# Performance work log

Hardware: AMD Instinct MI355X
Metric: run time of the kernel (lower is better)

The kernel has to match this reference:

```python
import jax, jax.numpy as jnp
import numpy as np

B, N, D, DS, LAT, FD, NF = 2, 384, 128, 3, 256, 1, 2
NPOS = DS * (2 * 5 + 1)  # 3 + 3*2*5 = 33
FREQS = np.linspace(1.0, 32.0, 5)  # torch.linspace(1, 2**5, 5)
EPS = 1e-5


def _bn(x, g, b):
    # BatchNorm1d, train-mode batch stats: normalize per channel over (batch, points)
    m = jnp.mean(x, axis=(0, 1))
    v = jnp.var(x, axis=(0, 1))
    return (x - m) * jax.lax.rsqrt(v + EPS) * g + b


def _tblock(xyz4, f, Wq, Wk, Wv, Wg1, bg1, Wg2, bg2, Wpe, bpe, g, b):
    # group_all=True full vector attention. f: [B,n,D], xyz4: [B,n,3]
    q = f @ Wq.T
    k = f @ Wk.T
    v = f @ Wv.T
    # knn_xyz gathered under no_grad in torch -> stop_gradient on the key side
    pd = xyz4[:, :, None] - jax.lax.stop_gradient(xyz4)[:, None]  # [B,n,n,3]
    parts = [pd]
    for fr in FREQS:
        parts.append(jnp.sin(pd * fr))
        parts.append(jnp.cos(pd * fr))
    pos = jnp.concatenate(parts, axis=-1) @ Wpe.T + bpe  # [B,n,n,D]
    edges = q[:, :, None] - k[:, None] + pos  # [B,n,n,D]
    h = jax.nn.relu(edges @ Wg1.T + bg1)
    attn = jax.nn.softmax(h @ Wg2.T + bg2, axis=-2)  # softmax over neighbor axis
    res = jnp.sum(attn * (v[:, None] + pos), axis=2)  # einsum bmnf,bmnf->bmf
    return _bn(res + f, g, b)


def setup_inputs() -> dict:
    key = jax.random.key(0)
    ks = iter(jax.random.split(key, 40))
    def rn(shape, s=0.05):
        return jax.random.normal(next(ks), shape, dtype=jnp.float32) * s
    z = lambda *s: jnp.zeros(s, jnp.float32)
    o = lambda *s: jnp.ones(s, jnp.float32)
    nb = NF + 1  # begin block + nfinal blocks
    return {
        "xyz": jax.random.normal(next(ks), (B, N, DS), dtype=jnp.float32),
        "feats": jax.random.normal(next(ks), (B, N, FD), dtype=jnp.float32),
        "enc_W": rn((D, FD)), "enc_b": z(D),
        "tb_Wq": rn((nb, D, D)), "tb_Wk": rn((nb, D, D)), "tb_Wv": rn((nb, D, D)),
        "tb_Wg1": rn((nb, D, D)), "tb_bg1": z(nb, D),
        "tb_Wg2": rn((nb, D, D)), "tb_bg2": z(nb, D),
        "tb_Wpe": rn((nb, D, NPOS)), "tb_bpe": z(nb, D),
        "tb_gamma": o(nb, D), "tb_beta": z(nb, D),
        "em_W1": rn((NF, D, D)), "em_b1": z(NF, D),
        "em_W2": rn((NF, D, D)), "em_b2": z(NF, D),
        "em_gamma": o(NF, D), "em_beta": z(NF, D),
        "fcf_W1": rn((LAT, D)), "fcf_b1": z(LAT),
        "fcf_W2": rn((LAT, LAT)), "fcf_b2": z(LAT),
    }


def reference(xyz, feats, enc_W, enc_b, tb_Wq, tb_Wk, tb_Wv, tb_Wg1, tb_bg1,
              tb_Wg2, tb_bg2, tb_Wpe, tb_bpe, tb_gamma, tb_beta,
              em_W1, em_b1, em_W2, em_b2, em_gamma, em_beta,
              fcf_W1, fcf_b1, fcf_W2, fcf_b2):
    f = feats @ enc_W.T + enc_b  # enc_feats
    x4 = xyz * 4.0
    for i in range(NF + 1):  # i=0: transformer_begin; i>=1: final transformers
        f = _tblock(x4, f, tb_Wq[i], tb_Wk[i], tb_Wv[i], tb_Wg1[i], tb_bg1[i],
                    tb_Wg2[i], tb_bg2[i], tb_Wpe[i], tb_bpe[i], tb_gamma[i], tb_beta[i])
        if i > 0:
            j = i - 1  # ElementwiseMLP: bn(x + relu(conv2(relu(conv1(x)))))
            y = jax.nn.relu(f @ em_W1[j].T + em_b1[j])
            y = jax.nn.relu(y @ em_W2[j].T + em_b2[j])
            f = _bn(f + y, em_gamma[j], em_beta[j])
    e = jax.nn.relu(f @ fcf_W1.T + fcf_b1) @ fcf_W2.T + fcf_b2
    return jnp.max(e, axis=1)  # lat_rep [B, lat_dim]
```

## Files before the change

kernel.cpp:

```cpp
#include <hip/hip_runtime.h>
#include <hip/hip_bf16.h>

#define B_ 2
#define N_ 384
#define D_ 128
#define LAT_ 256
#define NPOS_ 33
#define ROWS_ (B_*N_)
#define NT_ 64
#define ITERS_ (N_/NT_)

typedef __attribute__((ext_vector_type(8))) short bf16x8;
typedef __attribute__((ext_vector_type(4))) float f32x4;

#define MFMA(a,b,c) __builtin_amdgcn_mfma_f32_16x16x32_bf16((a),(b),(c),0,0,0)

__device__ __forceinline__ unsigned short f2bf(float x) {
    unsigned int u = __float_as_uint(x);
    u += 0x7FFFu + ((u >> 16) & 1u);
    return (unsigned short)(u >> 16);
}

__device__ __forceinline__ float bn_apply(float x, const float* stats, const float* gam,
                                          const float* bet, int d) {
    float s  = stats[d], sq = stats[128 + d];
    float mean = s * (1.f/ROWS_);
    float var  = sq * (1.f/ROWS_) - mean*mean;
    return (x - mean) * rsqrtf(var + 1e-5f) * gam[d] + bet[d];
}

__global__ __launch_bounds__(256) void enc_kernel(const float* __restrict__ feats,
                           const float* __restrict__ W,
                           const float* __restrict__ bias,
                           float* __restrict__ f) {
    int i = blockIdx.x*256 + threadIdx.x;
    if (i >= ROWS_*D_) return;
    int r = i >> 7, d = i & 127;
    f[i] = feats[r]*W[d] + bias[d];
}

__global__ __launch_bounds__(128) void qkv_kernel(const float* __restrict__ graw,
    const float* __restrict__ stats, const float* __restrict__ gam, const float* __restrict__ bet,
    int use_stats,
    const float* __restrict__ Wq, const float* __restrict__ Wk, const float* __restrict__ Wv,
    float* __restrict__ q, float* __restrict__ k, float* __restrict__ v) {
    __shared__ float row[D_];
    int r = blockIdx.x, d = threadIdx.x;
    float x = graw[r*D_+d];
    if (use_stats) x = bn_apply(x, stats, gam, bet, d);
    row[d] = x;
    __syncthreads();
    float aq=0.f, ak=0.f, av=0.f;
    #pragma unroll 4
    for (int e4=0;e4<D_/4;e4++){
        float4 wq = *(const float4*)(Wq + d*D_ + e4*4);
        float4 wk = *(const float4*)(Wk + d*D_ + e4*4);
        float4 wv = *(const float4*)(Wv + d*D_ + e4*4);
        float x0=row[e4*4+0], x1=row[e4*4+1], x2=row[e4*4+2], x3=row[e4*4+3];
        aq += wq.x*x0 + wq.y*x1 + wq.z*x2 + wq.w*x3;
        ak += wk.x*x0 + wk.y*x1 + wk.z*x2 + wk.w*x3;
        av += wv.x*x0 + wv.y*x1 + wv.z*x2 + wv.w*x3;
    }
    q[r*D_+d]=aq; k[r*D_+d]=ak; v[r*D_+d]=av;
}

__global__ __launch_bounds__(512) void attn_mfma_kernel(
    const float* __restrict__ xyz, const float* __restrict__ graw,
    const float* __restrict__ stats_in, const float* __restrict__ gam_in,
    const float* __restrict__ bet_in, int use_stats,
    const float* __restrict__ qb, const float* __restrict__ kb, const float* __restrict__ vb,
    const float* __restrict__ Wpe, const float* __restrict__ bpe,
    const float* __restrict__ Wg1, const float* __restrict__ bg1,
    const float* __restrict__ Wg2, const float* __restrict__ bg2,
    float* __restrict__ gout, float* __restrict__ stats_out)
{
    __shared__ unsigned short sParts[NT_*64];
    __shared__ unsigned short sX[NT_*128];
    __shared__ unsigned short sH[NT_*128];
    __shared__ float sRed[4*128];

    const int t   = threadIdx.x;
    const int w   = t >> 6;
    const int l   = t & 63;
    const int lr  = l & 15;
    const int lg  = l >> 4;
    const int rb2 = w >> 2;
    const int ct0 = (w & 3) * 2;

    const int row  = blockIdx.x;
    const int b    = row / N_;
    const int brow = b * N_;

    bf16x8 bWg1[2][4], bWg2[2][4], bWpe[2][2];
    float  bpe_c[2], bg1_c[2], bg2_c[2], q_c[2];

    #pragma unroll
    for (int ct = 0; ct < 2; ++ct) {
        const int dout = (ct0 + ct) * 16 + lr;
        #pragma unroll
        for (int kt = 0; kt < 4; ++kt) {
            const float* p1 = Wg1 + dout * D_ + kt * 32 + lg * 8;
            const float* p2 = Wg2 + dout * D_ + kt * 32 + lg * 8;
            float4 a0 = *(const float4*)(p1);
            float4 a1 = *(const float4*)(p1 + 4);
            float4 c0 = *(const float4*)(p2);
            float4 c1 = *(const float4*)(p2 + 4);
            bf16x8 v1, v2;
            v1[0]=(short)f2bf(a0.x); v1[1]=(short)f2bf(a0.y); v1[2]=(short)f2bf(a0.z); v1[3]=(short)f2bf(a0.w);
            v1[4]=(short)f2bf(a1.x); v1[5]=(short)f2bf(a1.y); v1[6]=(short)f2bf(a1.z); v1[7]=(short)f2bf(a1.w);
            v2[0]=(short)f2bf(c0.x); v2[1]=(short)f2bf(c0.y); v2[2]=(short)f2bf(c0.z); v2[3]=(short)f2bf(c0.w);
            v2[4]=(short)f2bf(c1.x); v2[5]=(short)f2bf(c1.y); v2[6]=(short)f2bf(c1.z); v2[7]=(short)f2bf(c1.w);
            bWg1[ct][kt] = v1;
            bWg2[ct][kt] = v2;
        }
        #pragma unroll
        for (int kt = 0; kt < 2; ++kt) {
            bf16x8 vv;
            #pragma unroll
            for (int e = 0; e < 8; ++e) {
                const int p = kt*32 + lg*8 + e;
                const float x = (p < NPOS_) ? Wpe[dout*NPOS_ + p] : 0.f;
                vv[e] = (short)f2bf(x);
            }
            bWpe[ct][kt] = vv;
        }
        bpe_c[ct] = bpe[dout];
        bg1_c[ct] = bg1[dout];
        bg2_c[ct] = bg2[dout];
        q_c[ct]   = qb[row*D_ + dout];
    }

    const float x4m0 = 4.f*xyz[row*3+0];
    const float x4m1 = 4.f*xyz[row*3+1];
    const float x4m2 = 4.f*xyz[row*3+2];

    for (int i = t; i < NT_*64/2; i += 512) ((unsigned int*)sParts)[i] = 0u;
    __syncthreads();

    auto partsgen = [&](int n0) {
        const int rr = t >> 3, j = t & 7;
        const int nr = (brow + n0 + rr) * 3;
        const float pd0 = x4m0 - 4.f*xyz[nr+0];
        const float pd1 = x4m1 - 4.f*xyz[nr+1];
        const float pd2 = x4m2 - 4.f*xyz[nr+2];
        auto pval = [&](int p) -> float {
            if (p < 3) return p==0?pd0:(p==1?pd1:pd2);
            const int qq = p - 3;
            const int fi = qq / 6;
            int rem = qq - fi*6;
            bool is_sin = true;
            if (rem >= 3) { rem -= 3; is_sin = false; }
            const float pdj = rem==0?pd0:(rem==1?pd1:pd2);
            const float fr = fi==0?1.f:(fi==1?8.75f:(fi==2?16.5f:(fi==3?24.25f:32.f)));
            const float a = pdj * fr;
            return is_sin ? __sinf(a) : __cosf(a);
        };
        const int sw = (rr & 7) << 3;
        #pragma unroll
        for (int k8 = 0; k8 < 4; ++k8) {
            const int p = j + k8*8;
            sParts[(rr*64 + p) ^ sw] = f2bf(pval(p));
        }
        if (j == 0) sParts[(rr*64 + 32) ^ sw] = f2bf(pval(32));
    };

    float kreg[2][2][4], vreg[2][2][4];
    auto loadK = [&](int n0) {
        #pragma unroll
        for (int rt = 0; rt < 2; ++rt)
        #pragma unroll
        for (int ct = 0; ct < 2; ++ct) {
            const int d = (ct0 + ct)*16 + lr;
            #pragma unroll
            for (int r = 0; r < 4; ++r) {
                const int rr = rb2*32 + rt*16 + lg*4 + r;
                kreg[rt][ct][r] = kb[(brow + n0 + rr)*D_ + d];
            }
        }
    };
    auto loadV = [&](int n0) {
        #pragma unroll
        for (int rt = 0; rt < 2; ++rt)
        #pragma unroll
        for (int ct = 0; ct < 2; ++ct) {
            const int d = (ct0 + ct)*16 + lr;
            #pragma unroll
            for (int r = 0; r < 4; ++r) {
                const int rr = rb2*32 + rt*16 + lg*4 + r;
                vreg[rt][ct][r] = vb[(brow + n0 + rr)*D_ + d];
            }
        }
    };

    f32x4 pos[2][2];
    auto posedges = [&]() {
        #pragma unroll
        for (int rt = 0; rt < 2; ++rt)
        #pragma unroll
        for (int ct = 0; ct < 2; ++ct) {
            f32x4 acc = {0.f, 0.f, 0.f, 0.f};
            #pragma unroll
            for (int kt = 0; kt < 2; ++kt) {
                const int r16 = rb2*32 + rt*16 + lr;
                const int idx = (r16*64 + kt*32 + lg*8) ^ ((r16 & 7) << 3);
                bf16x8 a = *(const bf16x8*)&sParts[idx];
                acc = MFMA(a, bWpe[ct][kt], acc);
            }
            #pragma unroll
            for (int r = 0; r < 4; ++r) acc[r] += bpe_c[ct];
            pos[rt][ct] = acc;
        }
        #pragma unroll
        for (int rt = 0; rt < 2; ++rt)
        #pragma unroll
        for (int ct = 0; ct < 2; ++ct) {
            const int d = (ct0 + ct)*16 + lr;
            #pragma unroll
            for (int r = 0; r < 4; ++r) {
                const int rr = rb2*32 + rt*16 + lg*4 + r;
                const float e = pos[rt][ct][r] + q_c[ct] - kreg[rt][ct][r];
                sX[(rr*128 + d) ^ ((rr & 7) << 3)] = f2bf(e);
            }
        }
    };

    partsgen(0);
    __syncthreads();
    loadK(0);
    posedges();
    __syncthreads();

    float res_p[2] = {0.f, 0.f}, s_p[2] = {0.f, 0.f};

    for (int it = 0; it < ITERS_; ++it) {
        const int n0 = it * NT_;
        const bool more = (it < ITERS_ - 1);

        loadV(n0);
        f32x4 hacc[2][2];
        #pragma unroll
        for (int rt = 0; rt < 2; ++rt) {
            hacc[rt][0] = (f32x4){bg1_c[0], bg1_c[0], bg1_c[0], bg1_c[0]};
            hacc[rt][1] = (f32x4){bg1_c[1], bg1_c[1], bg1_c[1], bg1_c[1]};
            #pragma unroll
            for (int kt = 0; kt < 4; ++kt) {
                const int r16 = rb2*32 + rt*16 + lr;
                const int idx = (r16*128 + kt*32 + lg*8) ^ ((r16 & 7) << 3);
                bf16x8 a = *(const bf16x8*)&sX[idx];
                hacc[rt][0] = MFMA(a, bWg1[0][kt], hacc[rt][0]);
                hacc[rt][1] = MFMA(a, bWg1[1][kt], hacc[rt][1]);
            }
        }
        #pragma unroll
        for (int rt = 0; rt < 2; ++rt)
        #pragma unroll
        for (int ct = 0; ct < 2; ++ct) {
            const int d = (ct0 + ct)*16 + lr;
            #pragma unroll
            for (int r = 0; r < 4; ++r) {
                const int rr = rb2*32 + rt*16 + lg*4 + r;
                sH[(rr*128 + d) ^ ((rr & 7) << 3)] = f2bf(fmaxf(hacc[rt][ct][r], 0.f));
            }
        }
        __syncthreads();

        if (more) loadK(n0 + NT_);
        f32x4 lacc[2][2];
        #pragma unroll
        for (int rt = 0; rt < 2; ++rt) {
            lacc[rt][0] = (f32x4){bg2_c[0], bg2_c[0], bg2_c[0], bg2_c[0]};
            lacc[rt][1] = (f32x4){bg2_c[1], bg2_c[1], bg2_c[1], bg2_c[1]};
            #pragma unroll
            for (int kt = 0; kt < 4; ++kt) {
                const int r16 = rb2*32 + rt*16 + lr;
                const int idx = (r16*128 + kt*32 + lg*8) ^ ((r16 & 7) << 3);
                bf16x8 a = *(const bf16x8*)&sH[idx];
                lacc[rt][0] = MFMA(a, bWg2[0][kt], lacc[rt][0]);
                lacc[rt][1] = MFMA(a, bWg2[1][kt], lacc[rt][1]);
            }
        }
        #pragma unroll
        for (int rt = 0; rt < 2; ++rt)
        #pragma unroll
        for (int ct = 0; ct < 2; ++ct) {
            #pragma unroll
            for (int r = 0; r < 4; ++r) {
                const float wgt = __expf(lacc[rt][ct][r]);
                const float vp  = vreg[rt][ct][r] + pos[rt][ct][r];
                res_p[ct] += wgt * vp;
                s_p[ct]   += wgt;
            }
        }
        if (more) partsgen(n0 + NT_);
        __syncthreads();

        if (more) {
            posedges();
            __syncthreads();
        }
    }

    #pragma unroll
    for (int ct = 0; ct < 2; ++ct) {
        #pragma unroll
        for (int off = 16; off < 64; off <<= 1) {
            res_p[ct] += __shfl_xor(res_p[ct], off, 64);
            s_p[ct]   += __shfl_xor(s_p[ct], off, 64);
        }
    }
    if (lg == 0) {
        #pragma unroll
        for (int ct = 0; ct < 2; ++ct) {
            const int d = (ct0 + ct)*16 + lr;
            sRed[(rb2*2+0)*128 + d] = res_p[ct];
            sRed[(rb2*2+1)*128 + d] = s_p[ct];
        }
    }
    __syncthreads();
    if (t < D_) {
        const float rsum = sRed[t]       + sRed[2*128 + t];
        const float ssum = sRed[128 + t] + sRed[3*128 + t];
        float fres = graw[row*D_ + t];
        if (use_stats) fres = bn_apply(fres, stats_in, gam_in, bet_in, t);
        const float val = rsum / ssum + fres;
        gout[row*D_ + t] = val;
        atomicAdd(&stats_out[t], val);
        atomicAdd(&stats_out[128 + t], val*val);
    }
}

__global__ __launch_bounds__(128) void em_kernel(const float* __restrict__ graw,
    const float* __restrict__ stats_in, const float* __restrict__ gam_in, const float* __restrict__ bet_in,
    const float* __restrict__ W1, const float* __restrict__ b1,
    const float* __restrict__ W2, const float* __restrict__ b2,
    float* __restrict__ gout, float* __restrict__ stats_out)
{
    __shared__ float row[D_], y1[D_];
    int r = blockIdx.x, d = threadIdx.x;
    float fn = bn_apply(graw[r*D_+d], stats_in, gam_in, bet_in, d);
    row[d] = fn; __syncthreads();
    float a = b1[d];
    #pragma unroll 4
    for (int e4=0;e4<D_/4;e4++){
        float4 w = *(const float4*)(W1 + d*D_ + e4*4);
        a += w.x*row[e4*4+0] + w.y*row[e4*4+1] + w.z*row[e4*4+2] + w.w*row[e4*4+3];
    }
    y1[d] = fmaxf(a,0.f); __syncthreads();
    float a2 = b2[d];
    #pragma unroll 4
    for (int e4=0;e4<D_/4;e4++){
        float4 w = *(const float4*)(W2 + d*D_ + e4*4);
        a2 += w.x*y1[e4*4+0] + w.y*y1[e4*4+1] + w.z*y1[e4*4+2] + w.w*y1[e4*4+3];
    }
    a2 = fmaxf(a2,0.f);
    const float g2 = fn + a2;
    gout[r*D_+d] = g2;
    atomicAdd(&stats_out[d], g2);
    atomicAdd(&stats_out[128+d], g2*g2);
}

__global__ __launch_bounds__(256) void final_kernel(const float* __restrict__ graw,
    const float* __restrict__ stats_in, const float* __restrict__ gam_in, const float* __restrict__ bet_in,
    const float* __restrict__ W1, const float* __restrict__ b1,
    const float* __restrict__ W2, const float* __restrict__ b2,
    float* __restrict__ e_ws)
{
    __shared__ float row[D_];
    __shared__ float h1[LAT_];
    int r = blockIdx.x, t = threadIdx.x;
    if (t < D_) row[t] = bn_apply(graw[r*D_+t], stats_in, gam_in, bet_in, t);
    __syncthreads();
    float a = b1[t];
    #pragma unroll 4
    for (int e4=0;e4<D_/4;e4++){
        float4 w = *(const float4*)(W1 + t*D_ + e4*4);
        a += w.x*row[e4*4+0] + w.y*row[e4*4+1] + w.z*row[e4*4+2] + w.w*row[e4*4+3];
    }
    h1[t] = fmaxf(a,0.f);
    __syncthreads();
    float a2 = b2[t];
    #pragma unroll 4
    for (int e4=0;e4<LAT_/4;e4++){
        float4 w = *(const float4*)(W2 + t*LAT_ + e4*4);
        a2 += w.x*h1[e4*4+0] + w.y*h1[e4*4+1] + w.z*h1[e4*4+2] + w.w*h1[e4*4+3];
    }
    e_ws[r*LAT_+t] = a2;
}

__global__ __launch_bounds__(256) void maxred_kernel(const float* __restrict__ e_ws,
                                                     float* __restrict__ out)
{
    int b = blockIdx.x, l = threadIdx.x;
    float m = -INFINITY;
    #pragma unroll 8
    for (int n=0;n<N_;n++) m = fmaxf(m, e_ws[(b*N_+n)*LAT_+l]);
    out[b*LAT_+l] = m;
}

extern "C" void kernel_launch(void* const* d_in, const int* in_sizes, int n_in,
                              void* d_out, int out_size, void* d_ws, size_t ws_size,
                              hipStream_t stream) {
    (void)in_sizes; (void)n_in; (void)out_size; (void)ws_size;
    const float* xyz    = (const float*)d_in[0];
    const float* feats  = (const float*)d_in[1];
    const float* enc_W  = (const float*)d_in[2];
    const float* enc_b  = (const float*)d_in[3];
    const float* tb_Wq  = (const float*)d_in[4];
    const float* tb_Wk  = (const float*)d_in[5];
    const float* tb_Wv  = (const float*)d_in[6];
    const float* tb_Wg1 = (const float*)d_in[7];
    const float* tb_bg1 = (const float*)d_in[8];
    const float* tb_Wg2 = (const float*)d_in[9];
    const float* tb_bg2 = (const float*)d_in[10];
    const float* tb_Wpe = (const float*)d_in[11];
    const float* tb_bpe = (const float*)d_in[12];
    const float* tb_gamma = (const float*)d_in[13];
    const float* tb_beta  = (const float*)d_in[14];
    const float* em_W1  = (const float*)d_in[15];
    const float* em_b1  = (const float*)d_in[16];
    const float* em_W2  = (const float*)d_in[17];
    const float* em_b2  = (const float*)d_in[18];
    const float* em_gamma = (const float*)d_in[19];
    const float* em_beta  = (const float*)d_in[20];
    const float* fcf_W1 = (const float*)d_in[21];
    const float* fcf_b1 = (const float*)d_in[22];
    const float* fcf_W2 = (const float*)d_in[23];
    const float* fcf_b2 = (const float*)d_in[24];
    float* out = (float*)d_out;

    float* ws   = (float*)d_ws;
    float* buf0 = ws;
    float* buf1 = buf0 + ROWS_*D_;
    float* qbuf = buf1 + ROWS_*D_;
    float* kbuf = qbuf + ROWS_*D_;
    float* vbuf = kbuf + ROWS_*D_;
    float* ebuf = vbuf + ROWS_*D_;
    float* stats = ebuf + ROWS_*LAT_;
    float* sA0 = stats;
    float* sA1 = stats + 256;
    float* sE1 = stats + 512;
    float* sA2 = stats + 768;
    float* sE2 = stats + 1024;

    hipMemsetAsync(stats, 0, 5*256*sizeof(float), stream);

    enc_kernel<<<(ROWS_*D_+255)/256, 256, 0, stream>>>(feats, enc_W, enc_b, buf0);

    const float* gz = tb_gamma;
    qkv_kernel<<<ROWS_, 128, 0, stream>>>(buf0, gz, gz, gz, 0,
                                          tb_Wq, tb_Wk, tb_Wv, qbuf, kbuf, vbuf);
    attn_mfma_kernel<<<ROWS_, 512, 0, stream>>>(xyz, buf0, gz, gz, gz, 0,
        qbuf, kbuf, vbuf,
        tb_Wpe, tb_bpe, tb_Wg1, tb_bg1, tb_Wg2, tb_bg2, buf1, sA0);
    qkv_kernel<<<ROWS_, 128, 0, stream>>>(buf1, sA0, tb_gamma, tb_beta, 1,
                                          tb_Wq + 1*D_*D_, tb_Wk + 1*D_*D_, tb_Wv + 1*D_*D_,
                                          qbuf, kbuf, vbuf);
    attn_mfma_kernel<<<ROWS_, 512, 0, stream>>>(xyz, buf1, sA0, tb_gamma, tb_beta, 1,
        qbuf, kbuf, vbuf,
        tb_Wpe + 1*D_*NPOS_, tb_bpe + 1*D_, tb_Wg1 + 1*D_*D_, tb_bg1 + 1*D_,
        tb_Wg2 + 1*D_*D_, tb_bg2 + 1*D_, buf0, sA1);
    em_kernel<<<ROWS_, 128, 0, stream>>>(buf0, sA1, tb_gamma + 1*D_, tb_beta + 1*D_,
                                         em_W1, em_b1, em_W2, em_b2, buf1, sE1);
    qkv_kernel<<<ROWS_, 128, 0, stream>>>(buf1, sE1, em_gamma, em_beta, 1,
                                          tb_Wq + 2*D_*D_, tb_Wk + 2*D_*D_, tb_Wv + 2*D_*D_,
                                          qbuf, kbuf, vbuf);
    attn_mfma_kernel<<<ROWS_, 512, 0, stream>>>(xyz, buf1, sE1, em_gamma, em_beta, 1,
        qbuf, kbuf, vbuf,
        tb_Wpe + 2*D_*NPOS_, tb_bpe + 2*D_, tb_Wg1 + 2*D_*D_, tb_bg1 + 2*D_,
        tb_Wg2 + 2*D_*D_, tb_bg2 + 2*D_, buf0, sA2);
    em_kernel<<<ROWS_, 128, 0, stream>>>(buf0, sA2, tb_gamma + 2*D_, tb_beta + 2*D_,
                                         em_W1 + 1*D_*D_, em_b1 + 1*D_,
                                         em_W2 + 1*D_*D_, em_b2 + 1*D_, buf1, sE2);
    final_kernel<<<ROWS_, 256, 0, stream>>>(buf1, sE2, em_gamma + 1*D_, em_beta + 1*D_,
                                            fcf_W1, fcf_b1, fcf_W2, fcf_b2, ebuf);
    maxred_kernel<<<B_, 256, 0, stream>>>(ebuf, out);
}
```

Measured before the change: 607.6 us.

## Factor positional sin/cos encoding via angle addition and precompute per-point features

Uses the angle-addition identities to split sin/cos(f*(xm-xn)) into per-point sin/cos features of the neighbour, computed once by a new prep kernel, and folds the query-side terms into per-row MFMA weights. This removes per-tile transcendental generation and one barrier from the attention loop. K and V are stored as bf16 to halve their loads, and the K prefetch moves earlier. The qkv, em and final kernels now process four rows per block to reuse weight loads. Accuracy may change slightly because the folded weights are rounded to bf16 after combining with the query-side sin/cos.

```diff
diff --git a/kernel.cpp b/kernel.cpp
--- a/kernel.cpp
+++ b/kernel.cpp
@@ -20,6 +20,9 @@
     u += 0x7FFFu + ((u >> 16) & 1u);
     return (unsigned short)(u >> 16);
 }
+__device__ __forceinline__ float bf2f(unsigned short u) {
+    return __uint_as_float(((unsigned int)u) << 16);
+}
 
 __device__ __forceinline__ float bn_apply(float x, const float* stats, const float* gam,
                                           const float* bet, int d) {
@@ -27,6 +30,23 @@
     float mean = s * (1.f/ROWS_);
     float var  = sq * (1.f/ROWS_) - mean*mean;
     return (x - mean) * rsqrtf(var + 1e-5f) * gam[d] + bet[d];
+}
+
+__global__ __launch_bounds__(256) void fprep_kernel(const float* __restrict__ xyz,
+                                                    unsigned short* __restrict__ gF) {
+    int i = blockIdx.x*256 + threadIdx.x;
+    if (i >= ROWS_*64) return;
+    int n = i >> 6, q = i & 63;
+    float val;
+    if (q == 0) val = 1.f;
+    else if (q < 4) val = 4.f*xyz[n*3 + (q-1)];
+    else if (q < 34) {
+        int u = q-4, fi = u/6, rem = u - fi*6, j = rem >> 1;
+        const float fr = fi==0?1.f:(fi==1?8.75f:(fi==2?16.5f:(fi==3?24.25f:32.f)));
+        float a = fr*4.f*xyz[n*3+j];
+        val = (rem & 1) ? __sinf(a) : __cosf(a);
+    } else val = 0.f;
+    gF[n*64 + (q ^ ((n & 7) << 3))] = f2bf(val);
 }
 
 __global__ __launch_bounds__(256) void enc_kernel(const float* __restrict__ feats,
@@ -43,38 +63,51 @@
     const float* __restrict__ stats, const float* __restrict__ gam, const float* __restrict__ bet,
     int use_stats,
     const float* __restrict__ Wq, const float* __restrict__ Wk, const float* __restrict__ Wv,
-    float* __restrict__ q, float* __restrict__ k, float* __restrict__ v) {
-    __shared__ float row[D_];
-    int r = blockIdx.x, d = threadIdx.x;
-    float x = graw[r*D_+d];
-    if (use_stats) x = bn_apply(x, stats, gam, bet, d);
-    row[d] = x;
-    __syncthreads();
-    float aq=0.f, ak=0.f, av=0.f;
+    float* __restrict__ q, unsigned short* __restrict__ k16, unsigned short* __restrict__ v16) {
+    __shared__ float rows[4][D_];
+    const int r0 = blockIdx.x*4, d = threadIdx.x;
+    #pragma unroll
+    for (int rr = 0; rr < 4; ++rr) {
+        float x = graw[(r0+rr)*D_ + d];
+        if (use_stats) x = bn_apply(x, stats, gam, bet, d);
+        rows[rr][d] = x;
+    }
+    __syncthreads();
+    float aq[4] = {0,0,0,0}, ak[4] = {0,0,0,0}, av[4] = {0,0,0,0};
     #pragma unroll 4
-    for (int e4=0;e4<D_/4;e4++){
+    for (int e4 = 0; e4 < D_/4; ++e4) {
         float4 wq = *(const float4*)(Wq + d*D_ + e4*4);
         float4 wk = *(const float4*)(Wk + d*D_ + e4*4);
         float4 wv = *(const float4*)(Wv + d*D_ + e4*4);
-        float x0=row[e4*4+0], x1=row[e4*4+1], x2=row[e4*4+2], x3=row[e4*4+3];
-        aq += wq.x*x0 + wq.y*x1 + wq.z*x2 + wq.w*x3;
-        ak += wk.x*x0 + wk.y*x1 + wk.z*x2 + wk.w*x3;
-        av += wv.x*x0 + wv.y*x1 + wv.z*x2 + wv.w*x3;
-    }
-    q[r*D_+d]=aq; k[r*D_+d]=ak; v[r*D_+d]=av;
+        #pragma unroll
+        for (int rr = 0; rr < 4; ++rr) {
+            float4 x = *(const float4*)&rows[rr][e4*4];
+            aq[rr] += wq.x*x.x + wq.y*x.y + wq.z*x.z + wq.w*x.w;
+            ak[rr] += wk.x*x.x + wk.y*x.y + wk.z*x.z + wk.w*x.w;
+            av[rr] += wv.x*x.x + wv.y*x.y + wv.z*x.z + wv.w*x.w;
+        }
+    }
+    #pragma unroll
+    for (int rr = 0; rr < 4; ++rr) {
+        q[(r0+rr)*D_ + d]   = aq[rr];
+        k16[(r0+rr)*D_ + d] = f2bf(ak[rr]);
+        v16[(r0+rr)*D_ + d] = f2bf(av[rr]);
+    }
 }
 
 __global__ __launch_bounds__(512) void attn_mfma_kernel(
     const float* __restrict__ xyz, const float* __restrict__ graw,
     const float* __restrict__ stats_in, const float* __restrict__ gam_in,
     const float* __restrict__ bet_in, int use_stats,
-    const float* __restrict__ qb, const float* __restrict__ kb, const float* __restrict__ vb,
+    const float* __restrict__ qb,
+    const unsigned short* __restrict__ kb, const unsigned short* __restrict__ vb,
+    const unsigned short* __restrict__ gF,
     const float* __restrict__ Wpe, const float* __restrict__ bpe,
     const float* __restrict__ Wg1, const float* __restrict__ bg1,
     const float* __restrict__ Wg2, const float* __restrict__ bg2,
     float* __restrict__ gout, float* __restrict__ stats_out)
 {
-    __shared__ unsigned short sParts[NT_*64];
+    __shared__ unsigned short sF[NT_*64];
     __shared__ unsigned short sX[NT_*128];
     __shared__ unsigned short sH[NT_*128];
     __shared__ float sRed[4*128];
@@ -91,8 +124,43 @@
     const int b    = row / N_;
     const int brow = b * N_;
 
-    bf16x8 bWg1[2][4], bWg2[2][4], bWpe[2][2];
-    float  bpe_c[2], bg1_c[2], bg2_c[2], q_c[2];
+    uint4 fst = *(const uint4*)(gF + (size_t)brow*64 + t*8);
+
+    float kreg[2][2][4], vreg[2][2][4];
+    auto loadK = [&](int n0) {
+        #pragma unroll
+        for (int rt = 0; rt < 2; ++rt)
+        #pragma unroll
+        for (int ct = 0; ct < 2; ++ct) {
+            const int d = (ct0 + ct)*16 + lr;
+            #pragma unroll
+            for (int r = 0; r < 4; ++r) {
+                const int rr = rb2*32 + rt*16 + lg*4 + r;
+                kreg[rt][ct][r] = bf2f(kb[(brow + n0 + rr)*D_ + d]);
+            }
+        }
+    };
+    auto loadV = [&](int n0) {
+        #pragma unroll
+        for (int rt = 0; rt < 2; ++rt)
+        #pragma unroll
+        for (int ct = 0; ct < 2; ++ct) {
+            const int d = (ct0 + ct)*16 + lr;
+            #pragma unroll
+            for (int r = 0; r < 4; ++r) {
+                const int rr = rb2*32 + rt*16 + lg*4 + r;
+                vreg[rt][ct][r] = bf2f(vb[(brow + n0 + rr)*D_ + d]);
+            }
+        }
+    };
+    loadK(0);
+
+    bf16x8 bWg1[2][4], bWg2[2][4], bG[2][2];
+    float  bg1_c[2], bg2_c[2], q_c[2];
+
+    const float xm0 = 4.f*xyz[row*3+0];
+    const float xm1 = 4.f*xyz[row*3+1];
+    const float xm2 = 4.f*xyz[row*3+2];
 
     #pragma unroll
     for (int ct = 0; ct < 2; ++ct) {
@@ -113,85 +181,35 @@
             bWg1[ct][kt] = v1;
             bWg2[ct][kt] = v2;
         }
+        const float* wrow = Wpe + dout*NPOS_;
+        float bias = bpe[dout] + wrow[0]*xm0 + wrow[1]*xm1 + wrow[2]*xm2;
         #pragma unroll
         for (int kt = 0; kt < 2; ++kt) {
-            bf16x8 vv;
+            bf16x8 g;
             #pragma unroll
             for (int e = 0; e < 8; ++e) {
-                const int p = kt*32 + lg*8 + e;
-                const float x = (p < NPOS_) ? Wpe[dout*NPOS_ + p] : 0.f;
-                vv[e] = (short)f2bf(x);
-            }
-            bWpe[ct][kt] = vv;
-        }
-        bpe_c[ct] = bpe[dout];
+                const int qq = kt*32 + lg*8 + e;
+                float val;
+                if (qq == 0) val = bias;
+                else if (qq < 4) val = -wrow[qq-1];
+                else if (qq < 34) {
+                    const int u = qq - 4, fi = u/6, rem = u - fi*6, j = rem >> 1;
+                    const float Ws = wrow[3 + 6*fi + j];
+                    const float Wc = wrow[3 + 6*fi + 3 + j];
+                    const float fr = fi==0?1.f:(fi==1?8.75f:(fi==2?16.5f:(fi==3?24.25f:32.f)));
+                    const float am = fr * (j==0?xm0:(j==1?xm1:xm2));
+                    const float sm = __sinf(am), cm = __cosf(am);
+                    val = (rem & 1) ? (Wc*sm - Ws*cm) : (Ws*sm + Wc*cm);
+                } else val = 0.f;
+                g[e] = (short)f2bf(val);
+            }
+            bG[ct][kt] = g;
+        }
         bg1_c[ct] = bg1[dout];
         bg2_c[ct] = bg2[dout];
         q_c[ct]   = qb[row*D_ + dout];
     }
 
-    const float x4m0 = 4.f*xyz[row*3+0];
-    const float x4m1 = 4.f*xyz[row*3+1];
-    const float x4m2 = 4.f*xyz[row*3+2];
-
-    for (int i = t; i < NT_*64/2; i += 512) ((unsigned int*)sParts)[i] = 0u;
-    __syncthreads();
-
-    auto partsgen = [&](int n0) {
-        const int rr = t >> 3, j = t & 7;
-        const int nr = (brow + n0 + rr) * 3;
-        const float pd0 = x4m0 - 4.f*xyz[nr+0];
-        const float pd1 = x4m1 - 4.f*xyz[nr+1];
-        const float pd2 = x4m2 - 4.f*xyz[nr+2];
-        auto pval = [&](int p) -> float {
-            if (p < 3) return p==0?pd0:(p==1?pd1:pd2);
-            const int qq = p - 3;
-            const int fi = qq / 6;
-            int rem = qq - fi*6;
-            bool is_sin = true;
-            if (rem >= 3) { rem -= 3; is_sin = false; }
-            const float pdj = rem==0?pd0:(rem==1?pd1:pd2);
-            const float fr = fi==0?1.f:(fi==1?8.75f:(fi==2?16.5f:(fi==3?24.25f:32.f)));
-            const float a = pdj * fr;
-            return is_sin ? __sinf(a) : __cosf(a);
-        };
-        const int sw = (rr & 7) << 3;
-        #pragma unroll
-        for (int k8 = 0; k8 < 4; ++k8) {
-            const int p = j + k8*8;
-            sParts[(rr*64 + p) ^ sw] = f2bf(pval(p));
-        }
-        if (j == 0) sParts[(rr*64 + 32) ^ sw] = f2bf(pval(32));
-    };
-
-    float kreg[2][2][4], vreg[2][2][4];
-    auto loadK = [&](int n0) {
-        #pragma unroll
-        for (int rt = 0; rt < 2; ++rt)
-        #pragma unroll
-        for (int ct = 0; ct < 2; ++ct) {
-            const int d = (ct0 + ct)*16 + lr;
-            #pragma unroll
-            for (int r = 0; r < 4; ++r) {
-                const int rr = rb2*32 + rt*16 + lg*4 + r;
-                kreg[rt][ct][r] = kb[(brow + n0 + rr)*D_ + d];
-            }
-        }
-    };
-    auto loadV = [&](int n0) {
-        #pragma unroll
-        for (int rt = 0; rt < 2; ++rt)
-        #pragma unroll
-        for (int ct = 0; ct < 2; ++ct) {
-            const int d = (ct0 + ct)*16 + lr;
-            #pragma unroll
-            for (int r = 0; r < 4; ++r) {
-                const int rr = rb2*32 + rt*16 + lg*4 + r;
-                vreg[rt][ct][r] = vb[(brow + n0 + rr)*D_ + d];
-            }
-        }
-    };
-
     f32x4 pos[2][2];
     auto posedges = [&]() {
         #pragma unroll
@@ -203,11 +221,9 @@
             for (int kt = 0; kt < 2; ++kt) {
                 const int r16 = rb2*32 + rt*16 + lr;
                 const int idx = (r16*64 + kt*32 + lg*8) ^ ((r16 & 7) << 3);
-                bf16x8 a = *(const bf16x8*)&sParts[idx];
-                acc = MFMA(a, bWpe[ct][kt], acc);
-            }
-            #pragma unroll
-            for (int r = 0; r < 4; ++r) acc[r] += bpe_c[ct];
+                bf16x8 a = *(const bf16x8*)&sF[idx];
+                acc = MFMA(a, bG[ct][kt], acc);
+            }
             pos[rt][ct] = acc;
         }
         #pragma unroll
@@ -224,9 +240,8 @@
         }
     };
 
-    partsgen(0);
-    __syncthreads();
-    loadK(0);
+    *(uint4*)&sF[t*8] = fst;
+    __syncthreads();
     posedges();
     __syncthreads();
 
@@ -236,6 +251,10 @@
         const int n0 = it * NT_;
         const bool more = (it < ITERS_ - 1);
 
+        if (more) {
+            fst = *(const uint4*)(gF + (size_t)(brow + n0 + NT_)*64 + t*8);
+            loadK(n0 + NT_);
+        }
         loadV(n0);
         f32x4 hacc[2][2];
         #pragma unroll
@@ -262,9 +281,9 @@
                 sH[(rr*128 + d) ^ ((rr & 7) << 3)] = f2bf(fmaxf(hacc[rt][ct][r], 0.f));
             }
         }
+        if (more) *(uint4*)&sF[t*8] = fst;
         __syncthreads();
 
-        if (more) loadK(n0 + NT_);
         f32x4 lacc[2][2];
         #pragma unroll
         for (int rt = 0; rt < 2; ++rt) {
@@ -291,9 +310,6 @@
                 s_p[ct]   += wgt;
             }
         }
-        if (more) partsgen(n0 + NT_);
-        __syncthreads();
-
         if (more) {
             posedges();
             __syncthreads();
@@ -335,28 +351,45 @@
     const float* __restrict__ W2, const float* __restrict__ b2,
     float* __restrict__ gout, float* __restrict__ stats_out)
 {
-    __shared__ float row[D_], y1[D_];
-    int r = blockIdx.x, d = threadIdx.x;
-    float fn = bn_apply(graw[r*D_+d], stats_in, gam_in, bet_in, d);
-    row[d] = fn; __syncthreads();
-    float a = b1[d];
+    __shared__ float rows[4][D_], y1[4][D_];
+    const int r0 = blockIdx.x*4, d = threadIdx.x;
+    float fn[4];
+    #pragma unroll
+    for (int rr = 0; rr < 4; ++rr) {
+        fn[rr] = bn_apply(graw[(r0+rr)*D_ + d], stats_in, gam_in, bet_in, d);
+        rows[rr][d] = fn[rr];
+    }
+    __syncthreads();
+    float a[4] = {b1[d], b1[d], b1[d], b1[d]};
     #pragma unroll 4
-    for (int e4=0;e4<D_/4;e4++){
+    for (int e4 = 0; e4 < D_/4; ++e4) {
         float4 w = *(const float4*)(W1 + d*D_ + e4*4);
-        a += w.x*row[e4*4+0] + w.y*row[e4*4+1] + w.z*row[e4*4+2] + w.w*row[e4*4+3];
-    }
-    y1[d] = fmaxf(a,0.f); __syncthreads();
-    float a2 = b2[d];
+        #pragma unroll
+        for (int rr = 0; rr < 4; ++rr) {
+            float4 x = *(const float4*)&rows[rr][e4*4];
+            a[rr] += w.x*x.x + w.y*x.y + w.z*x.z + w.w*x.w;
+        }
+    }
+    #pragma unroll
+    for (int rr = 0; rr < 4; ++rr) y1[rr][d] = fmaxf(a[rr], 0.f);
+    __syncthreads();
+    float a2[4] = {b2[d], b2[d], b2[d], b2[d]};
     #pragma unroll 4
-    for (int e4=0;e4<D_/4;e4++){
+    for (int e4 = 0; e4 < D_/4; ++e4) {
         float4 w = *(const float4*)(W2 + d*D_ + e4*4);
-        a2 += w.x*y1[e4*4+0] + w.y*y1[e4*4+1] + w.z*y1[e4*4+2] + w.w*y1[e4*4+3];
-    }
-    a2 = fmaxf(a2,0.f);
-    const float g2 = fn + a2;
-    gout[r*D_+d] = g2;
-    atomicAdd(&stats_out[d], g2);
-    atomicAdd(&stats_out[128+d], g2*g2);
+        #pragma unroll
+        for (int rr = 0; rr < 4; ++rr) {
+            float4 x = *(const float4*)&y1[rr][e4*4];
+            a2[rr] += w.x*x.x + w.y*x.y + w.z*x.z + w.w*x.w;
+        }
+    }
+    #pragma unroll
+    for (int rr = 0; rr < 4; ++rr) {
+        const float g2 = fn[rr] + fmaxf(a2[rr], 0.f);
+        gout[(r0+rr)*D_ + d] = g2;
+        atomicAdd(&stats_out[d], g2);
+        atomicAdd(&stats_out[128+d], g2*g2);
+    }
 }
 
 __global__ __launch_bounds__(256) void final_kernel(const float* __restrict__ graw,
@@ -365,26 +398,39 @@
     const float* __restrict__ W2, const float* __restrict__ b2,
     float* __restrict__ e_ws)
 {
-    __shared__ float row[D_];
-    __shared__ float h1[LAT_];
-    int r = blockIdx.x, t = threadIdx.x;
-    if (t < D_) row[t] = bn_apply(graw[r*D_+t], stats_in, gam_in, bet_in, t);
-    __syncthreads();
-    float a = b1[t];
+    __shared__ float rows[4][D_];
+    __shared__ float h1[4][LAT_];
+    const int r0 = blockIdx.x*4, t = threadIdx.x;
+    for (int i = t; i < 4*D_; i += 256) {
+        const int rr = i >> 7, d = i & 127;
+        rows[rr][d] = bn_apply(graw[(r0+rr)*D_ + d], stats_in, gam_in, bet_in, d);
+    }
+    __syncthreads();
+    float a[4] = {b1[t], b1[t], b1[t], b1[t]};
     #pragma unroll 4
-    for (int e4=0;e4<D_/4;e4++){
+    for (int e4 = 0; e4 < D_/4; ++e4) {
         float4 w = *(const float4*)(W1 + t*D_ + e4*4);
-        a += w.x*row[e4*4+0] + w.y*row[e4*4+1] + w.z*row[e4*4+2] + w.w*row[e4*4+3];
-    }
-    h1[t] = fmaxf(a,0.f);
-    __syncthreads();
-    float a2 = b2[t];
+        #pragma unroll
+        for (int rr = 0; rr < 4; ++rr) {
+            float4 x = *(const float4*)&rows[rr][e4*4];
+            a[rr] += w.x*x.x + w.y*x.y + w.z*x.z + w.w*x.w;
+        }
+    }
+    #pragma unroll
+    for (int rr = 0; rr < 4; ++rr) h1[rr][t] = fmaxf(a[rr], 0.f);
+    __syncthreads();
+    float a2[4] = {b2[t], b2[t], b2[t], b2[t]};
     #pragma unroll 4
-    for (int e4=0;e4<LAT_/4;e4++){
+    for (int e4 = 0; e4 < LAT_/4; ++e4) {
         float4 w = *(const float4*)(W2 + t*LAT_ + e4*4);
-        a2 += w.x*h1[e4*4+0] + w.y*h1[e4*4+1] + w.z*h1[e4*4+2] + w.w*h1[e4*4+3];
-    }
-    e_ws[r*LAT_+t] = a2;
+        #pragma unroll
+        for (int rr = 0; rr < 4; ++rr) {
+            float4 x = *(const float4*)&h1[rr][e4*4];
+            a2[rr] += w.x*x.x + w.y*x.y + w.z*x.z + w.w*x.w;
+        }
+    }
+    #pragma unroll
+    for (int rr = 0; rr < 4; ++rr) e_ws[(r0+rr)*LAT_ + t] = a2[rr];
 }
 
 __global__ __launch_bounds__(256) void maxred_kernel(const float* __restrict__ e_ws,
@@ -432,46 +478,48 @@
     float* buf0 = ws;
     float* buf1 = buf0 + ROWS_*D_;
     float* qbuf = buf1 + ROWS_*D_;
-    float* kbuf = qbuf + ROWS_*D_;
-    float* vbuf = kbuf + ROWS_*D_;
-    float* ebuf = vbuf + ROWS_*D_;
+    float* ebuf = qbuf + ROWS_*D_;
     float* stats = ebuf + ROWS_*LAT_;
     float* sA0 = stats;
     float* sA1 = stats + 256;
     float* sE1 = stats + 512;
     float* sA2 = stats + 768;
     float* sE2 = stats + 1024;
+    unsigned short* kbuf = (unsigned short*)(stats + 5*256);
+    unsigned short* vbuf = kbuf + ROWS_*D_;
+    unsigned short* gF   = vbuf + ROWS_*D_;
 
     hipMemsetAsync(stats, 0, 5*256*sizeof(float), stream);
 
+    fprep_kernel<<<(ROWS_*64+255)/256, 256, 0, stream>>>(xyz, gF);
     enc_kernel<<<(ROWS_*D_+255)/256, 256, 0, stream>>>(feats, enc_W, enc_b, buf0);
 
     const float* gz = tb_gamma;
-    qkv_kernel<<<ROWS_, 128, 0, stream>>>(buf0, gz, gz, gz, 0,
-                                          tb_Wq, tb_Wk, tb_Wv, qbuf, kbuf, vbuf);
+    qkv_kernel<<<ROWS_/4, 128, 0, stream>>>(buf0, gz, gz, gz, 0,
+                                            tb_Wq, tb_Wk, tb_Wv, qbuf, kbuf, vbuf);
     attn_mfma_kernel<<<ROWS_, 512, 0, stream>>>(xyz, buf0, gz, gz, gz, 0,
-        qbuf, kbuf, vbuf,
+        qbuf, kbuf, vbuf, gF,
         tb_Wpe, tb_bpe, tb_Wg1, tb_bg1, tb_Wg2, tb_bg2, buf1, sA0);
-    qkv_kernel<<<ROWS_, 128, 0, stream>>>(buf1, sA0, tb_gamma, tb_beta, 1,
-                                          tb_Wq + 1*D_*D_, tb_Wk + 1*D_*D_, tb_Wv + 1*D_*D_,
-                                          qbuf, kbuf, vbuf);
+    qkv_kernel<<<ROWS_/4, 128, 0, stream>>>(buf1, sA0, tb_gamma, tb_beta, 1,
+                                            tb_Wq + 1*D_*D_, tb_Wk + 1*D_*D_, tb_Wv + 1*D_*D_,
+                                            qbuf, kbuf, vbuf);
     attn_mfma_kernel<<<ROWS_, 512, 0, stream>>>(xyz, buf1, sA0, tb_gamma, tb_beta, 1,
-        qbuf, kbuf, vbuf,
+        qbuf, kbuf, vbuf, gF,
         tb_Wpe + 1*D_*NPOS_, tb_bpe + 1*D_, tb_Wg1 + 1*D_*D_, tb_bg1 + 1*D_,
         tb_Wg2 + 1*D_*D_, tb_bg2 + 1*D_, buf0, sA1);
-    em_kernel<<<ROWS_, 128, 0, stream>>>(buf0, sA1, tb_gamma + 1*D_, tb_beta + 1*D_,
-                                         em_W1, em_b1, em_W2, em_b2, buf1, sE1);
-    qkv_kernel<<<ROWS_, 128, 0, stream>>>(buf1, sE1, em_gamma, em_beta, 1,
-                                          tb_Wq + 2*D_*D_, tb_Wk + 2*D_*D_, tb_Wv + 2*D_*D_,
-                                          qbuf, kbuf, vbuf);
+    em_kernel<<<ROWS_/4, 128, 0, stream>>>(buf0, sA1, tb_gamma + 1*D_, tb_beta + 1*D_,
+                                           em_W1, em_b1, em_W2, em_b2, buf1, sE1);
+    qkv_kernel<<<ROWS_/4, 128, 0, stream>>>(buf1, sE1, em_gamma, em_beta, 1,
+                                            tb_Wq + 2*D_*D_, tb_Wk + 2*D_*D_, tb_Wv + 2*D_*D_,
+                                            qbuf, kbuf, vbuf);
     attn_mfma_kernel<<<ROWS_, 512, 0, stream>>>(xyz, buf1, sE1, em_gamma, em_beta, 1,
-        qbuf, kbuf, vbuf,
+        qbuf, kbuf, vbuf, gF,
         tb_Wpe + 2*D_*NPOS_, tb_bpe + 2*D_, tb_Wg1 + 2*D_*D_, tb_bg1 + 2*D_,
         tb_Wg2 + 2*D_*D_, tb_bg2 + 2*D_, buf0, sA2);
-    em_kernel<<<ROWS_, 128, 0, stream>>>(buf0, sA2, tb_gamma + 2*D_, tb_beta + 2*D_,
-                                         em_W1 + 1*D_*D_, em_b1 + 1*D_,
-                                         em_W2 + 1*D_*D_, em_b2 + 1*D_, buf1, sE2);
-    final_kernel<<<ROWS_, 256, 0, stream>>>(buf1, sE2, em_gamma + 1*D_, em_beta + 1*D_,
-                                            fcf_W1, fcf_b1, fcf_W2, fcf_b2, ebuf);
+    em_kernel<<<ROWS_/4, 128, 0, stream>>>(buf0, sA2, tb_gamma + 2*D_, tb_beta + 2*D_,
+                                           em_W1 + 1*D_*D_, em_b1 + 1*D_,
+                                           em_W2 + 1*D_*D_, em_b2 + 1*D_, buf1, sE2);
+    final_kernel<<<ROWS_/4, 256, 0, stream>>>(buf1, sE2, em_gamma + 1*D_, em_beta + 1*D_,
+                                              fcf_W1, fcf_b1, fcf_W2, fcf_b2, ebuf);
     maxred_kernel<<<B_, 256, 0, stream>>>(ebuf, out);
 }
```

Result: slower. 689.3 us (+13.4%).
